# Kernel optimization log

Measured on AMD Instinct MI355X. Metric: run time of the kernel, lower is better.

Reference implementation:

```python
import jax, jax.numpy as jnp
import numpy as np

N = 50000      # nodes
E = 800000     # edges (before self loops)
F_IN = 128     # input feature dim
H = 2          # attention heads
C = 64         # hidden channels per head (H*C = 128 = layer-2 input dim)
G = 64         # graphs in batch
OUT = 10       # out_channels
NEG_SLOPE = 0.2  # PyG GATConv default leaky relu slope


def setup_inputs() -> dict:
    key = jax.random.key(0)
    ks = jax.random.split(key, 16)
    sc = lambda f: np.float32(1.0 / np.sqrt(f))
    inp = {
        "x": jax.random.normal(ks[0], (N, F_IN), jnp.float32),
        "edge_index": jax.random.randint(ks[1], (2, E), 0, N, dtype=jnp.int32),
        "batch": jnp.sort(jax.random.randint(ks[2], (N,), 0, G, dtype=jnp.int32)),
        # GATConv layer 1 (lazy (-1,-1): separate src/dst projections)
        "Ws1": jax.random.normal(ks[3], (F_IN, H * C), jnp.float32) * sc(F_IN),
        "Wd1": jax.random.normal(ks[4], (F_IN, H * C), jnp.float32) * sc(F_IN),
        "as1": jax.random.normal(ks[5], (H, C), jnp.float32) * sc(C),
        "ad1": jax.random.normal(ks[6], (H, C), jnp.float32) * sc(C),
        "b1": jnp.zeros((H * C,), jnp.float32),
        # GATConv layer 2 (input dim = H*C = 128)
        "Ws2": jax.random.normal(ks[7], (H * C, H * C), jnp.float32) * sc(H * C),
        "Wd2": jax.random.normal(ks[8], (H * C, H * C), jnp.float32) * sc(H * C),
        "as2": jax.random.normal(ks[9], (H, C), jnp.float32) * sc(C),
        "ad2": jax.random.normal(ks[10], (H, C), jnp.float32) * sc(C),
        "b2": jnp.zeros((H * C,), jnp.float32),
        # final linear
        "Wl": jax.random.normal(ks[11], (H * C, OUT), jnp.float32) * sc(H * C),
        "bl": jnp.zeros((OUT,), jnp.float32),
    }
    return inp


def gat_conv(x, src, dst, Ws, Wd, att_s, att_d, b):
    # x: [N, F]; src/dst: [E'] (self loops already included)
    n = x.shape[0]
    xs = (x @ Ws).reshape(n, H, C)          # source-side projection
    xd = (x @ Wd).reshape(n, H, C)          # dest-side projection
    a_s = jnp.einsum('nhc,hc->nh', xs, att_s)   # [N, H]
    a_d = jnp.einsum('nhc,hc->nh', xd, att_d)   # [N, H]
    e = a_s[src] + a_d[dst]                      # [E', H]
    e = jnp.where(e > 0, e, NEG_SLOPE * e)       # leaky_relu
    # softmax over incoming edges per destination node (every node has a self loop)
    m = jax.ops.segment_max(e, dst, num_segments=n)
    ew = jnp.exp(e - m[dst])
    denom = jax.ops.segment_sum(ew, dst, num_segments=n)
    alpha = ew / denom[dst]                      # [E', H]
    out = jax.ops.segment_sum(alpha[:, :, None] * xs[src], dst, num_segments=n)
    return out.reshape(n, H * C) + b


def reference(x, edge_index, batch, Ws1, Wd1, as1, ad1, b1, Ws2, Wd2, as2, ad2, b2, Wl, bl):
    # add self loops once (add_self_loops=True)
    loops = jnp.arange(N, dtype=edge_index.dtype)
    src = jnp.concatenate([edge_index[0], loops])
    dst = jnp.concatenate([edge_index[1], loops])

    h = jax.nn.relu(gat_conv(x, src, dst, Ws1, Wd1, as1, ad1, b1))
    h = jax.nn.relu(gat_conv(h, src, dst, Ws2, Wd2, as2, ad2, b2))

    # global_mean_pool over batch vector
    sums = jax.ops.segment_sum(h, batch, num_segments=G)
    cnt = jax.ops.segment_sum(jnp.ones((N,), h.dtype), batch, num_segments=G)
    pooled = sums / jnp.maximum(cnt, 1.0)[:, None]

    # dropout(p=0.5) is identity in eval mode
    return pooled @ Wl + bl
```

## Files before the change

### kernel.cpp

```cpp
#include <hip/hip_runtime.h>
#include <hip/hip_bf16.h>

#define N_NODES 50000
#define N_EDGES 800000
#define EP (N_EDGES + N_NODES)
#define N_GRAPHS 64
#define F_DIM 128
#define OUT_DIM 10
#define NB 391
#define NREP 64
#define SUBCAP 80
#define EIDS_CAP 2560

typedef __attribute__((ext_vector_type(8))) short short8;
typedef __attribute__((ext_vector_type(4))) float f32x4;

__device__ __forceinline__ unsigned int f2bf(float f) {
    unsigned int x; __builtin_memcpy(&x, &f, 4);
    return (x + 0x7fffu + ((x >> 16) & 1u)) >> 16;
}
__device__ __forceinline__ float bf2f(unsigned int u16) {
    unsigned int x = u16 << 16;
    float f; __builtin_memcpy(&f, &x, 4); return f;
}


__global__ __launch_bounds__(256) void prep_kernel(
    const float* __restrict__ W1, const float* __restrict__ W2,
    const float* __restrict__ Wd1, const float* __restrict__ ad1,
    const float* __restrict__ Wd2, const float* __restrict__ ad2,
    unsigned short* __restrict__ Wt1, unsigned short* __restrict__ Wt2,
    float* __restrict__ weffd1, float* __restrict__ weffd2,
    uint4* __restrict__ zero_bcur , uint4* __restrict__ zero_sums ) {
    int tid = blockIdx.x * 256 + threadIdx.x;
    if (tid < 6256) zero_bcur[tid] = make_uint4(0, 0, 0, 0);
    else if (tid < 6256 + 2048) zero_sums[tid - 6256] = make_uint4(0, 0, 0, 0);
    if (tid < 512) {
        const float* Wd = (tid < 256) ? Wd1 : Wd2;
        const float* ad = (tid < 256) ? ad1 : ad2;
        float* wout = (tid < 256) ? weffd1 : weffd2;
        int i = tid & 255, f = i >> 1, h = i & 1;
        const float4* wr = (const float4*)(Wd + f * 128 + h * 64);
        const float4* av = (const float4*)(ad + h * 64);
        float s = 0.f;
        #pragma unroll
        for (int c = 0; c < 16; ++c) {
            float4 w = wr[c], a = av[c];
            s += w.x*a.x + w.y*a.y + w.z*a.z + w.w*a.w;
        }
        wout[f * 2 + h] = s;
    }
    const float* W = (tid < 16384) ? W1 : W2;
    unsigned short* Wt = (tid < 16384) ? Wt1 : Wt2;
    int i = tid & 16383;
    int k = i >> 7, nn = i & 127;
    Wt[nn * 128 + k] = (unsigned short)f2bf(W[i]);
}


__global__ void scatter_kernel(const int* __restrict__ ei,
                               int* __restrict__ bcursor,
                               unsigned int* __restrict__ recs) {
    int e = blockIdx.x * blockDim.x + threadIdx.x;
    if (e >= EP) return;
    int src, dst;
    if (e < N_EDGES) { src = ei[e]; dst = ei[N_EDGES + e]; }
    else             { src = e - N_EDGES; dst = src; }
    int b = dst >> 7, dl = dst & 127;
    int rep = e & (NREP - 1);
    int pos = atomicAdd(&bcursor[rep * NB + b], 1);
    if (pos < SUBCAP)
        recs[((size_t)b * NREP + rep) * SUBCAP + pos] = ((unsigned)dl << 16) | (unsigned)src;
}

__global__ __launch_bounds__(256) void bucketize_kernel(
    const unsigned int* __restrict__ recs, const int* __restrict__ bcursor,
    unsigned short* __restrict__ eids, int2* __restrict__ rsre, int n) {
    __shared__ int ssub[NREP + 1];
    __shared__ int hist[128], excl[128], cur[128];
    __shared__ unsigned int srec[EIDS_CAP];
    int b = blockIdx.x, t = threadIdx.x;
    if (t < 128) { hist[t] = 0; cur[t] = 0; }
    if (t < NREP) {
        int c = bcursor[t * NB + b]; if (c > SUBCAP) c = SUBCAP;
        int incl = c;
        #pragma unroll
        for (int d = 1; d < 64; d <<= 1) { int o = __shfl_up(incl, d, 64); if (t >= d) incl += o; }
        ssub[t + 1] = incl;
        if (t == 0) ssub[0] = 0;
    }
    __syncthreads();
    int total = ssub[NREP]; if (total > EIDS_CAP) total = EIDS_CAP;
    const unsigned int* rb = recs + (size_t)b * NREP * SUBCAP;
    for (int i = t; i < total; i += 256) {
        int lo = 0, hi = NREP;
        while (lo + 1 < hi) { int mid = (lo + hi) >> 1; if (ssub[mid] <= i) lo = mid; else hi = mid; }
        unsigned int rec = rb[lo * SUBCAP + (i - ssub[lo])];
        srec[i] = rec;
        atomicAdd(&hist[rec >> 16], 1);
    }
    __syncthreads();
    if (t < 128) excl[t] = hist[t];
    __syncthreads();
    for (int off = 1; off < 128; off <<= 1) {
        int v = 0;
        if (t < 128 && t >= off) v = excl[t - off];
        __syncthreads();
        if (t < 128) excl[t] += v;
        __syncthreads();
    }
    int base = b * EIDS_CAP;
    if (t < 128) {
        int d = b * 128 + t;
        if (d < n) rsre[d] = make_int2(base + excl[t] - hist[t], base + excl[t]);
    }
    __syncthreads();
    for (int i = t; i < total; i += 256) {
        unsigned int rec = srec[i];
        int dl = rec >> 16;
        int pos = atomicAdd(&cur[dl], 1);
        eids[(size_t)base + (excl[dl] - hist[dl]) + pos] = (unsigned short)(rec & 0xffffu);
    }
}


__global__ __launch_bounds__(256) void gemm_fused_f32a_kernel(
    const float* __restrict__ A, const unsigned short* __restrict__ Wt,
    const float* __restrict__ att_s, const float* __restrict__ weffd,
    unsigned short* __restrict__ C, float* __restrict__ a_s, float* __restrict__ a_d, int n) {
    int t = threadIdx.x;
    int l = t & 63;
    int quad = l >> 4, lr = l & 15;
    int m0 = blockIdx.x * 64 + (t >> 6) * 16;
    int arow = m0 + lr; if (arow >= n) arow = n - 1;

    short8 afrag[4];
    float pd0 = 0.f, pd1 = 0.f;
    const float2* wd2 = (const float2*)weffd;
    #pragma unroll
    for (int kb = 0; kb < 4; ++kb) {
        const float4* ap = (const float4*)(A + (size_t)arow * 128 + kb * 32 + quad * 8);
        float4 a0 = ap[0], a1 = ap[1];
        int k0 = kb * 32 + quad * 8;
        float2 w0 = wd2[k0+0], w1 = wd2[k0+1], w2 = wd2[k0+2], w3 = wd2[k0+3];
        float2 w4 = wd2[k0+4], w5 = wd2[k0+5], w6 = wd2[k0+6], w7 = wd2[k0+7];
        pd0 += a0.x*w0.x + a0.y*w1.x + a0.z*w2.x + a0.w*w3.x
             + a1.x*w4.x + a1.y*w5.x + a1.z*w6.x + a1.w*w7.x;
        pd1 += a0.x*w0.y + a0.y*w1.y + a0.z*w2.y + a0.w*w3.y
             + a1.x*w4.y + a1.y*w5.y + a1.z*w6.y + a1.w*w7.y;
        short8 s;
        s[0] = (short)f2bf(a0.x); s[1] = (short)f2bf(a0.y);
        s[2] = (short)f2bf(a0.z); s[3] = (short)f2bf(a0.w);
        s[4] = (short)f2bf(a1.x); s[5] = (short)f2bf(a1.y);
        s[6] = (short)f2bf(a1.z); s[7] = (short)f2bf(a1.w);
        afrag[kb] = s;
    }
    pd0 += __shfl_xor(pd0, 16); pd0 += __shfl_xor(pd0, 32);
    pd1 += __shfl_xor(pd1, 16); pd1 += __shfl_xor(pd1, 32);
    if (l < 16 && m0 + lr < n) *(float2*)(a_d + (size_t)(m0 + lr) * 2) = make_float2(pd0, pd1);

    f32x4 acc[8] = {};
    #pragma unroll
    for (int nt = 0; nt < 8; ++nt) {
        #pragma unroll
        for (int kb = 0; kb < 4; ++kb) {
            short8 b = *(const short8*)(Wt + (size_t)(nt * 16 + lr) * 128 + kb * 32 + quad * 8);
            acc[nt] = __builtin_amdgcn_mfma_f32_16x16x32_bf16(afrag[kb], b, acc[nt], 0, 0, 0);
        }
    }
    float asv[8];
    #pragma unroll
    for (int nt = 0; nt < 8; ++nt) asv[nt] = att_s[nt * 16 + lr];
    float pa0[4] = {}, pa1[4] = {};
    #pragma unroll
    for (int nt = 0; nt < 8; ++nt)
        #pragma unroll
        for (int r = 0; r < 4; ++r) {
            if (nt < 4) pa0[r] += acc[nt][r] * asv[nt];
            else        pa1[r] += acc[nt][r] * asv[nt];
        }
    #pragma unroll
    for (int d = 1; d < 16; d <<= 1) {
        #pragma unroll
        for (int r = 0; r < 4; ++r) {
            pa0[r] += __shfl_xor(pa0[r], d);
            pa1[r] += __shfl_xor(pa1[r], d);
        }
    }
    if (lr == 0) {
        #pragma unroll
        for (int r = 0; r < 4; ++r) {
            int row = m0 + quad * 4 + r;
            if (row < n) *(float2*)(a_s + (size_t)row * 2) = make_float2(pa0[r], pa1[r]);
        }
    }
    #pragma unroll
    for (int nt = 0; nt < 8; ++nt)
        #pragma unroll
        for (int r = 0; r < 4; ++r) {
            int row = m0 + quad * 4 + r;
            if (row < n)
                C[(size_t)row * 128 + nt * 16 + lr] = (unsigned short)f2bf(acc[nt][r]);
        }
}

__global__ __launch_bounds__(256) void gemm_fused_bf16_kernel(
    const unsigned short* __restrict__ A, const unsigned short* __restrict__ Wt,
    const float* __restrict__ att_s, const float* __restrict__ weffd,
    unsigned short* __restrict__ C, float* __restrict__ a_s, float* __restrict__ a_d, int n) {
    int t = threadIdx.x;
    int l = t & 63;
    int quad = l >> 4, lr = l & 15;
    int m0 = blockIdx.x * 64 + (t >> 6) * 16;
    int arow = m0 + lr; if (arow >= n) arow = n - 1;

    short8 afrag[4];
    float pd0 = 0.f, pd1 = 0.f;
    const float2* wd2 = (const float2*)weffd;
    #pragma unroll
    for (int kb = 0; kb < 4; ++kb) {
        short8 s = *(const short8*)(A + (size_t)arow * 128 + kb * 32 + quad * 8);
        afrag[kb] = s;
        const unsigned int* u = (const unsigned int*)&s;
        int k0 = kb * 32 + quad * 8;
        #pragma unroll
        for (int d = 0; d < 4; ++d) {
            float x0 = __uint_as_float(u[d] << 16);
            float x1 = __uint_as_float(u[d] & 0xffff0000u);
            float2 wv0 = wd2[k0 + 2*d], wv1 = wd2[k0 + 2*d + 1];
            pd0 += x0 * wv0.x + x1 * wv1.x;
            pd1 += x0 * wv0.y + x1 * wv1.y;
        }
    }
    pd0 += __shfl_xor(pd0, 16); pd0 += __shfl_xor(pd0, 32);
    pd1 += __shfl_xor(pd1, 16); pd1 += __shfl_xor(pd1, 32);
    if (l < 16 && m0 + lr < n) *(float2*)(a_d + (size_t)(m0 + lr) * 2) = make_float2(pd0, pd1);

    f32x4 acc[8] = {};
    #pragma unroll
    for (int nt = 0; nt < 8; ++nt) {
        #pragma unroll
        for (int kb = 0; kb < 4; ++kb) {
            short8 b = *(const short8*)(Wt + (size_t)(nt * 16 + lr) * 128 + kb * 32 + quad * 8);
            acc[nt] = __builtin_amdgcn_mfma_f32_16x16x32_bf16(afrag[kb], b, acc[nt], 0, 0, 0);
        }
    }
    float asv[8];
    #pragma unroll
    for (int nt = 0; nt < 8; ++nt) asv[nt] = att_s[nt * 16 + lr];
    float pa0[4] = {}, pa1[4] = {};
    #pragma unroll
    for (int nt = 0; nt < 8; ++nt)
        #pragma unroll
        for (int r = 0; r < 4; ++r) {
            if (nt < 4) pa0[r] += acc[nt][r] * asv[nt];
            else        pa1[r] += acc[nt][r] * asv[nt];
        }
    #pragma unroll
    for (int d = 1; d < 16; d <<= 1) {
        #pragma unroll
        for (int r = 0; r < 4; ++r) {
            pa0[r] += __shfl_xor(pa0[r], d);
            pa1[r] += __shfl_xor(pa1[r], d);
        }
    }
    if (lr == 0) {
        #pragma unroll
        for (int r = 0; r < 4; ++r) {
            int row = m0 + quad * 4 + r;
            if (row < n) *(float2*)(a_s + (size_t)row * 2) = make_float2(pa0[r], pa1[r]);
        }
    }
    #pragma unroll
    for (int nt = 0; nt < 8; ++nt)
        #pragma unroll
        for (int r = 0; r < 4; ++r) {
            int row = m0 + quad * 4 + r;
            if (row < n)
                C[(size_t)row * 128 + nt * 16 + lr] = (unsigned short)f2bf(acc[nt][r]);
        }
}


__global__ __launch_bounds__(256) void aggregate_kernel(
    const int2* __restrict__ rsre, const unsigned short* __restrict__ eids,
    const float* __restrict__ a_s, const float* __restrict__ a_d,
    const unsigned int* __restrict__ xs32, const float* __restrict__ bias,
    unsigned int* __restrict__ out32, int n) {
    int wave = (int)((blockIdx.x * blockDim.x + threadIdx.x) >> 6);
    int lane = threadIdx.x & 63;
    if (wave >= n) return;
    int dstn = wave;
    int h    = lane >> 5;
    int j32  = lane & 31;
    int hoff = h << 5;
    int ch   = lane * 2;
    float2 advv = *(const float2*)(a_d + (size_t)dstn * 2);
    float adv = (h == 0) ? advv.x : advv.y;
    int2 rr = rsre[dstn];
    int row = rr.x, end = rr.y;

    float accA0 = 0.f, accA1 = 0.f, accB0 = 0.f, accB1 = 0.f, lsum = 0.f;
    for (int base = row; base < end; base += 32) {
        int rem = end - base;
        int k = rem < 32 ? rem : 32;
        int idx = base + (j32 < k ? j32 : k - 1);
        int eidv = (int)eids[idx];
        float2 as2 = *(const float2*)(a_s + (size_t)eidv * 2);
        float e = ((h == 0) ? as2.x : as2.y) + adv;
        e = (e > 0.f) ? e : 0.2f * e;
        float pme = (j32 < k) ? __expf(e) : 0.f;
        lsum += pme;
        int jb = 0;
        for (; jb + 4 <= k; jb += 4) {
            #pragma unroll
            for (int u = 0; u < 4; ++u) {
                int j = jb + u;
                int srcn = __shfl(eidv, j);
                float pj = __shfl(pme, j + hoff);
                unsigned int v = xs32[(size_t)srcn * 64 + lane];
                if (u & 1) {
                    accB0 += pj * __uint_as_float(v << 16);
                    accB1 += pj * __uint_as_float(v & 0xffff0000u);
                } else {
                    accA0 += pj * __uint_as_float(v << 16);
                    accA1 += pj * __uint_as_float(v & 0xffff0000u);
                }
            }
        }
        for (; jb < k; ++jb) {
            int srcn = __shfl(eidv, jb);
            float pj = __shfl(pme, jb + hoff);
            unsigned int v = xs32[(size_t)srcn * 64 + lane];
            accA0 += pj * __uint_as_float(v << 16);
            accA1 += pj * __uint_as_float(v & 0xffff0000u);
        }
    }
    #pragma unroll
    for (int d = 1; d <= 16; d <<= 1) lsum += __shfl_xor(lsum, d);
    float inv = 1.f / lsum;
    float o0 = fmaxf((accA0 + accB0) * inv + bias[ch], 0.f);
    float o1 = fmaxf((accA1 + accB1) * inv + bias[ch + 1], 0.f);
    out32[(size_t)dstn * 64 + lane] = f2bf(o0) | (f2bf(o1) << 16);
}


#define POOL_CHUNK 128

__global__ __launch_bounds__(256) void pool_partial_kernel(
    const unsigned short* __restrict__ Hf, const int* __restrict__ batch,
    float* __restrict__ sums, int n) {
    int t = threadIdx.x;
    int c = t & 127, half = t >> 7;
    int start = blockIdx.x * POOL_CHUNK;
    int end = min(start + POOL_CHUNK, n);
    float acc = 0.f;
    int cur = -1;
    for (int i = start + half; i < end; i += 2) {
        int g = batch[i];
        if (g != cur) {
            if (cur >= 0) atomicAdd(&sums[cur * 128 + c], acc);
            acc = 0.f; cur = g;
        }
        acc += bf2f(Hf[(size_t)i * 128 + c]);
    }
    if (cur >= 0) atomicAdd(&sums[cur * 128 + c], acc);
}

__global__ void final_linear_kernel(const float* __restrict__ sums,
                                    const int* __restrict__ batch,
                                    const float* __restrict__ Wl, const float* __restrict__ bl,
                                    float* __restrict__ out, int n) {
    int t = blockIdx.x * blockDim.x + threadIdx.x;
    if (t >= N_GRAPHS * OUT_DIM) return;
    int g = t / OUT_DIM, o = t % OUT_DIM;
    int lo = 0, hi = n;
    while (lo < hi) { int mid = (lo + hi) >> 1; if (batch[mid] < g) lo = mid + 1; else hi = mid; }
    int s0 = lo; hi = n;
    while (lo < hi) { int mid = (lo + hi) >> 1; if (batch[mid] < g + 1) lo = mid + 1; else hi = mid; }
    float cnt = (float)(lo - s0);
    float inv = 1.f / fmaxf(cnt, 1.f);
    float s = bl[o];
    for (int c = 0; c < 128; ++c) s += sums[g * 128 + c] * inv * Wl[c * OUT_DIM + o];
    out[g * OUT_DIM + o] = s;
}


extern "C" void kernel_launch(void* const* d_in, const int* in_sizes, int n_in,
                              void* d_out, int out_size, void* d_ws, size_t ws_size,
                              hipStream_t stream) {
    const float* x    = (const float*)d_in[0];
    const int*   ei   = (const int*)d_in[1];
    const int*   batch= (const int*)d_in[2];
    const float* Ws1  = (const float*)d_in[3];
    const float* Wd1  = (const float*)d_in[4];
    const float* as1  = (const float*)d_in[5];
    const float* ad1  = (const float*)d_in[6];
    const float* b1   = (const float*)d_in[7];
    const float* Ws2  = (const float*)d_in[8];
    const float* Wd2  = (const float*)d_in[9];
    const float* as2  = (const float*)d_in[10];
    const float* ad2  = (const float*)d_in[11];
    const float* b2   = (const float*)d_in[12];
    const float* Wl   = (const float*)d_in[13];
    const float* bl   = (const float*)d_in[14];
    float* out = (float*)d_out;

    char* p = (char*)d_ws;
    auto alloc = [&](size_t bytes) {
        void* r = (void*)p;
        p += (bytes + 255) & ~(size_t)255;
        return r;
    };
    int* bcursor  = (int*)alloc(sizeof(int) * NREP * NB);
    unsigned short* eids = (unsigned short*)alloc(sizeof(short) * (size_t)NB * EIDS_CAP);
    int2* rsre    = (int2*)alloc(sizeof(int2) * N_NODES);
    float* a_s    = (float*)alloc(sizeof(float) * N_NODES * 2);
    float* a_d    = (float*)alloc(sizeof(float) * N_NODES * 2);
    float* sums   = (float*)alloc(sizeof(float) * N_GRAPHS * 128);
    float* weffd1 = (float*)alloc(sizeof(float) * 128 * 2);
    float* weffd2 = (float*)alloc(sizeof(float) * 128 * 2);
    unsigned short* Wt1  = (unsigned short*)alloc(sizeof(short) * 128 * 128);
    unsigned short* Wt2  = (unsigned short*)alloc(sizeof(short) * 128 * 128);
    unsigned short* bufA = (unsigned short*)alloc(sizeof(short) * (size_t)N_NODES * F_DIM);
    unsigned short* bufB = (unsigned short*)alloc(sizeof(short) * (size_t)N_NODES * F_DIM);
    unsigned int* recs = (unsigned int*)bufA;

    prep_kernel<<<128, 256, 0, stream>>>(Ws1, Ws2, Wd1, ad1, Wd2, ad2,
                                         Wt1, Wt2, weffd1, weffd2,
                                         (uint4*)bcursor, (uint4*)sums);
    scatter_kernel<<<(EP + 255) / 256, 256, 0, stream>>>(ei, bcursor, recs);
    bucketize_kernel<<<NB, 256, 0, stream>>>(recs, bcursor, eids, rsre, N_NODES);

    const int gemm_grid = (N_NODES + 63) / 64;
    const int agg_grid  = (N_NODES + 3) / 4;

    gemm_fused_f32a_kernel<<<gemm_grid, 256, 0, stream>>>(x, Wt1, as1, weffd1,
                                                          bufA, a_s, a_d, N_NODES);
    aggregate_kernel<<<agg_grid, 256, 0, stream>>>(rsre, eids, a_s, a_d,
                                                   (const unsigned int*)bufA, b1,
                                                   (unsigned int*)bufB, N_NODES);

    gemm_fused_bf16_kernel<<<gemm_grid, 256, 0, stream>>>(bufB, Wt2, as2, weffd2,
                                                          bufA, a_s, a_d, N_NODES);
    aggregate_kernel<<<agg_grid, 256, 0, stream>>>(rsre, eids, a_s, a_d,
                                                   (const unsigned int*)bufA, b2,
                                                   (unsigned int*)bufB, N_NODES);

    pool_partial_kernel<<<(N_NODES + POOL_CHUNK - 1) / POOL_CHUNK, 256, 0, stream>>>(bufB, batch, sums, N_NODES);
    final_linear_kernel<<<(N_GRAPHS * OUT_DIM + 255) / 256, 256, 0, stream>>>(sums, batch, Wl, bl, out, N_NODES);
}
```

Baseline: 325.0 us.

## Block-local histogram scatter with bulk global atomics and implicit self loops

```diff
diff --git a/kernel.cpp b/kernel.cpp
--- a/kernel.cpp
+++ b/kernel.cpp
@@ -8,9 +8,11 @@
 #define F_DIM 128
 #define OUT_DIM 10
 #define NB 391
-#define NREP 64
-#define SUBCAP 80
+#define NREP 8
+#define SUBCAP 384
 #define EIDS_CAP 2560
+#define SC_EDGES 4096
+#define SC_BLOCKS ((N_EDGES + SC_EDGES - 1) / SC_EDGES)
 
 typedef __attribute__((ext_vector_type(8))) short short8;
 typedef __attribute__((ext_vector_type(4))) float f32x4;
@@ -33,8 +35,8 @@
     float* __restrict__ weffd1, float* __restrict__ weffd2,
     uint4* __restrict__ zero_bcur , uint4* __restrict__ zero_sums ) {
     int tid = blockIdx.x * 256 + threadIdx.x;
-    if (tid < 6256) zero_bcur[tid] = make_uint4(0, 0, 0, 0);
-    else if (tid < 6256 + 2048) zero_sums[tid - 6256] = make_uint4(0, 0, 0, 0);
+    if (tid < 782) zero_bcur[tid] = make_uint4(0, 0, 0, 0);
+    else if (tid < 782 + 2048) zero_sums[tid - 782] = make_uint4(0, 0, 0, 0);
     if (tid < 512) {
         const float* Wd = (tid < 256) ? Wd1 : Wd2;
         const float* ad = (tid < 256) ? ad1 : ad2;
@@ -58,19 +60,58 @@
 }
 
 
-__global__ void scatter_kernel(const int* __restrict__ ei,
-                               int* __restrict__ bcursor,
-                               unsigned int* __restrict__ recs) {
-    int e = blockIdx.x * blockDim.x + threadIdx.x;
-    if (e >= EP) return;
-    int src, dst;
-    if (e < N_EDGES) { src = ei[e]; dst = ei[N_EDGES + e]; }
-    else             { src = e - N_EDGES; dst = src; }
-    int b = dst >> 7, dl = dst & 127;
-    int rep = e & (NREP - 1);
-    int pos = atomicAdd(&bcursor[rep * NB + b], 1);
-    if (pos < SUBCAP)
-        recs[((size_t)b * NREP + rep) * SUBCAP + pos] = ((unsigned)dl << 16) | (unsigned)src;
+__global__ __launch_bounds__(1024) void scatter_kernel(const int* __restrict__ ei,
+                                                       int* __restrict__ bcursor,
+                                                       unsigned int* __restrict__ recs) {
+    __shared__ unsigned int srec[SC_EDGES];
+    __shared__ int hist[NB], lcur[NB], gpos[NB];
+    __shared__ int excl[512];
+    int t = threadIdx.x;
+    int base = blockIdx.x * SC_EDGES;
+    int rep = blockIdx.x & (NREP - 1);
+    for (int i = t; i < NB; i += 1024) { hist[i] = 0; lcur[i] = 0; }
+    __syncthreads();
+    unsigned int rec_[4]; int have[4];
+    #pragma unroll
+    for (int j = 0; j < 4; ++j) {
+        int i = base + j * 1024 + t;
+        have[j] = (i < N_EDGES);
+        if (have[j]) {
+            int src = ei[i], dst = ei[N_EDGES + i];
+            int b = dst >> 7;
+            rec_[j] = ((unsigned)b << 23) | ((unsigned)(dst & 127) << 16) | (unsigned)src;
+            atomicAdd(&hist[b], 1);
+        }
+    }
+    __syncthreads();
+    if (t < 512) excl[t] = (t < NB) ? hist[t] : 0;
+    __syncthreads();
+    for (int off = 1; off < 512; off <<= 1) {
+        int v = 0;
+        if (t < 512 && t >= off) v = excl[t - off];
+        __syncthreads();
+        if (t < 512) excl[t] += v;
+        __syncthreads();
+    }
+    if (t < NB && hist[t] > 0) gpos[t] = atomicAdd(&bcursor[rep * NB + t], hist[t]);
+    __syncthreads();
+    #pragma unroll
+    for (int j = 0; j < 4; ++j) {
+        if (have[j]) {
+            int b = rec_[j] >> 23;
+            int pos = atomicAdd(&lcur[b], 1);
+            srec[(excl[b] - hist[b]) + pos] = rec_[j];
+        }
+    }
+    __syncthreads();
+    int cnt = N_EDGES - base; if (cnt > SC_EDGES) cnt = SC_EDGES;
+    for (int i = t; i < cnt; i += 1024) {
+        unsigned int rec = srec[i];
+        int b = rec >> 23;
+        int gp = gpos[b] + (i - (excl[b] - hist[b]));
+        if (gp < SUBCAP)
+            recs[((size_t)b * NREP + rep) * SUBCAP + gp] = rec & 0x7fffffu;
+    }
 }
 
 __global__ __launch_bounds__(256) void bucketize_kernel(
@@ -80,25 +121,29 @@
     __shared__ int hist[128], excl[128], cur[128];
     __shared__ unsigned int srec[EIDS_CAP];
     int b = blockIdx.x, t = threadIdx.x;
+    int nvalid = n - b * 128; if (nvalid > 128) nvalid = 128;
     if (t < 128) { hist[t] = 0; cur[t] = 0; }
-    if (t < NREP) {
-        int c = bcursor[t * NB + b]; if (c > SUBCAP) c = SUBCAP;
-        int incl = c;
-        #pragma unroll
-        for (int d = 1; d < 64; d <<= 1) { int o = __shfl_up(incl, d, 64); if (t >= d) incl += o; }
-        ssub[t + 1] = incl;
-        if (t == 0) ssub[0] = 0;
-    }
-    __syncthreads();
-    int total = ssub[NREP]; if (total > EIDS_CAP) total = EIDS_CAP;
+    if (t == 0) {
+        int run = 0; ssub[0] = 0;
+        for (int r = 0; r < NREP; ++r) {
+            int c = bcursor[r * NB + b]; if (c > SUBCAP) c = SUBCAP;
+            run += c; ssub[r + 1] = run;
+        }
+    }
+    __syncthreads();
+    int total = ssub[NREP];
+    int maxsc = EIDS_CAP - 128;
+    if (total > maxsc) total = maxsc;
     const unsigned int* rb = recs + (size_t)b * NREP * SUBCAP;
     for (int i = t; i < total; i += 256) {
-        int lo = 0, hi = NREP;
-        while (lo + 1 < hi) { int mid = (lo + hi) >> 1; if (ssub[mid] <= i) lo = mid; else hi = mid; }
-        unsigned int rec = rb[lo * SUBCAP + (i - ssub[lo])];
+        int r = 0;
+        while (ssub[r + 1] <= i) ++r;
+        unsigned int rec = rb[r * SUBCAP + (i - ssub[r])];
         srec[i] = rec;
-        atomicAdd(&hist[rec >> 16], 1);
-    }
+        atomicAdd(&hist[(rec >> 16) & 127], 1);
+    }
+    __syncthreads();
+    if (t < nvalid) hist[t] += 1;
     __syncthreads();
     if (t < 128) excl[t] = hist[t];
     __syncthreads();
@@ -109,17 +154,19 @@
         if (t < 128) excl[t] += v;
         __syncthreads();
     }
-    int base = b * EIDS_CAP;
-    if (t < 128) {
-        int d = b * 128 + t;
-        if (d < n) rsre[d] = make_int2(base + excl[t] - hist[t], base + excl[t]);
+    int base2 = b * EIDS_CAP;
+    if (t < nvalid) {
+        int st = excl[t] - hist[t];
+        rsre[b * 128 + t] = make_int2(base2 + st, base2 + excl[t]);
+        eids[base2 + st] = (unsigned short)(b * 128 + t);
+        cur[t] = 1;
     }
     __syncthreads();
     for (int i = t; i < total; i += 256) {
         unsigned int rec = srec[i];
-        int dl = rec >> 16;
+        int dl = (rec >> 16) & 127;
         int pos = atomicAdd(&cur[dl], 1);
-        eids[(size_t)base + (excl[dl] - hist[dl]) + pos] = (unsigned short)(rec & 0xffffu);
+        eids[base2 + (excl[dl] - hist[dl]) + pos] = (unsigned short)(rec & 0xffffu);
     }
 }
 
@@ -429,7 +476,7 @@
     prep_kernel<<<128, 256, 0, stream>>>(Ws1, Ws2, Wd1, ad1, Wd2, ad2,
                                          Wt1, Wt2, weffd1, weffd2,
                                          (uint4*)bcursor, (uint4*)sums);
-    scatter_kernel<<<(EP + 255) / 256, 256, 0, stream>>>(ei, bcursor, recs);
+    scatter_kernel<<<SC_BLOCKS, 1024, 0, stream>>>(ei, bcursor, recs);
     bucketize_kernel<<<NB, 256, 0, stream>>>(recs, bcursor, eids, rsre, N_NODES);
 
     const int gemm_grid = (N_NODES + 63) / 64;
```

Result: faster. 277.6 us (-14.6%).
